# Optimization experiments

Hardware: AMD Instinct MI355X
Metric: run time of the kernel (lower is better)

## Reference

```python
import jax, jax.numpy as jnp
import numpy as np

B, C, H, W = 2, 256, 48, 48
KD = 256          # key_dim
CLS = 20          # num_classes
NT = H * W        # patch tokens in query
N = CLS + NT      # key length (cls tokens + patches)
HDS = 8           # num_heads
HD = C // HDS     # head_dim
SCALE = HD ** -0.5
MR = 0.3          # mask_ratio
EPS = 1e-5


def setup_inputs() -> dict:
    key = jax.random.key(0)
    ks = jax.random.split(key, 10)
    s = 0.02
    return {
        "x_query": jax.random.normal(ks[0], (B, C, H, W), jnp.float32),
        "x_key": jax.random.normal(ks[1], (B, N, KD), jnp.float32),
        "mask_u": jax.random.uniform(ks[2], (B, HDS, N, N), jnp.float32),
        "g1": jnp.ones((C,), jnp.float32), "be1": jnp.zeros((C,), jnp.float32),
        "g2": jnp.ones((KD,), jnp.float32), "be2": jnp.zeros((KD,), jnp.float32),
        "g3": jnp.ones((C,), jnp.float32), "be3": jnp.zeros((C,), jnp.float32),
        "Wq": jax.random.normal(ks[3], (C, C), jnp.float32) * s,
        "Wkv": jax.random.normal(ks[4], (KD, 2 * C), jnp.float32) * s,
        "Wcls": jax.random.normal(ks[5], (KD, C), jnp.float32) * s,
        "Wp": jax.random.normal(ks[6], (C, C), jnp.float32) * s,
        "bp": jnp.zeros((C,), jnp.float32),
        "W1": jax.random.normal(ks[7], (C, 4 * C), jnp.float32) * s,
        "bf1": jnp.zeros((4 * C,), jnp.float32),
        "W2": jax.random.normal(ks[8], (4 * C, C), jnp.float32) * s,
        "bf2": jnp.zeros((C,), jnp.float32),
    }


def _ln(x, g, b):
    m = jnp.mean(x, -1, keepdims=True)
    v = jnp.mean((x - m) ** 2, -1, keepdims=True)
    return (x - m) * jax.lax.rsqrt(v + EPS) * g + b


def reference(x_query, x_key, mask_u, g1, be1, g2, be2, g3, be3,
              Wq, Wkv, Wcls, Wp, bp, W1, bf1, W2, bf2):
    Bb, Cc, Hh, Ww = x_query.shape
    xq = x_query.transpose(0, 2, 3, 1).reshape(Bb, -1, Cc)  # [B, Nt, C]
    q_in = _ln(xq, g1, be1)
    k_in = _ln(x_key, g2, be2)
    # cross attention with cls-token prepend
    cls_t = k_in[:, :CLS] @ Wcls                      # [B, Cls, C]
    qcat = jnp.concatenate([cls_t, q_in @ Wq], 1)     # [B, Cls+Nt, C]
    M = qcat.shape[1]
    Nk = x_key.shape[1]
    q = qcat.reshape(Bb, M, HDS, HD).transpose(0, 2, 1, 3)        # [B,h,M,d]
    kv = (k_in @ Wkv).reshape(Bb, Nk, 2, HDS, HD).transpose(2, 0, 3, 1, 4)
    k, v = kv[0], kv[1]                                           # [B,h,N,d]
    attn = jnp.einsum('bhmd,bhnd->bhmn', q, k) * SCALE            # [B,h,M,N]
    # split softmax: cls columns and patch columns normalized separately
    attn = jnp.concatenate([
        jax.nn.softmax(attn[..., :CLS], axis=-1),
        jax.nn.softmax(attn[..., CLS:], axis=-1),
    ], axis=-1)
    # stochastic bernoulli(mask_ratio) mask -> -1e12, then re-softmax
    bern = (mask_u < MR).astype(attn.dtype)
    attn = jax.nn.softmax(attn + bern * (-1e12), axis=-1)
    x = jnp.einsum('bhmn,bhnd->bhmd', attn, v)
    x = x.transpose(0, 2, 1, 3).reshape(Bb, M, Cc)
    x = x @ Wp + bp
    x = x[:, CLS:]                                    # drop cls rows
    xq = xq + x                                       # residual 1
    h = jax.nn.gelu(_ln(xq, g3, be3) @ W1 + bf1, approximate=False)
    xq = xq + (h @ W2 + bf2)                          # residual 2 (MLP)
    return xq.transpose(0, 2, 1).reshape(Bb, Cc, Hh, Ww)
```

## Files before the change

### kernel.cpp

```cpp
#include <hip/hip_runtime.h>
#include <hip/hip_bf16.h>
#include <cstddef>

#define B_ 2
#define C_ 256
#define HW_ 2304
#define CLS_ 20
#define N_ 2324
#define HDS_ 8
#define HD_ 32
#define SCALE_F 0.17677669529663687f
#define MR_ 0.3f
#define EPS_ 1e-5f
#define NT64 37
#define NPAD 2368

typedef __attribute__((ext_vector_type(8))) short short8;
typedef __attribute__((ext_vector_type(4))) float f32x4;
typedef unsigned long long u64;

__device__ __forceinline__ short f2bf(float x) {
    union { __hip_bfloat16 b; short s; } u;
    u.b = __float2bfloat16(x);
    return u.s;
}
__device__ __forceinline__ u64 shfl_xor_u64(u64 v, int m) {
    unsigned lo = (unsigned)v, hi = (unsigned)(v >> 32);
    lo = (unsigned)__shfl_xor((int)lo, m, 64);
    hi = (unsigned)__shfl_xor((int)hi, m, 64);
    return ((u64)hi << 32) | lo;
}

__global__ __launch_bounds__(256) void wtrans_all_kernel(
    const float* __restrict__ Wq,  const float* __restrict__ Wkv,
    const float* __restrict__ Wp,  const float* __restrict__ W1,
    const float* __restrict__ W2,
    short* __restrict__ Wq_t, short* __restrict__ Wkv_t,
    short* __restrict__ Wp_t, short* __restrict__ W1_t,
    short* __restrict__ W2_t)
{
    __shared__ float S[32][33];
    int bid = blockIdx.x;
    const float* W; short* Wt; int K, Nn; float scale;
    if (bid < 64)       { W = Wq;  Wt = Wq_t;  K = 256;  Nn = 256;  scale = SCALE_F; }
    else if (bid < 192) { bid -= 64;  W = Wkv; Wt = Wkv_t; K = 256;  Nn = 512;  scale = 1.f; }
    else if (bid < 256) { bid -= 192; W = Wp;  Wt = Wp_t;  K = 256;  Nn = 256;  scale = 1.f; }
    else if (bid < 512) { bid -= 256; W = W1;  Wt = W1_t;  K = 256;  Nn = 1024; scale = 1.f; }
    else                { bid -= 512; W = W2;  Wt = W2_t;  K = 1024; Nn = 256;  scale = 1.f; }
    int nblk = Nn / 32;
    int n0 = (bid % nblk) * 32, k0 = (bid / nblk) * 32;
    int t = threadIdx.x;
    int nl = t & 31, kq = t >> 5;
    #pragma unroll
    for (int ii = 0; ii < 4; ++ii) {
        int k = kq + ii * 8;
        S[k][nl] = W[(size_t)(k0 + k) * Nn + n0 + nl] * scale;
    }
    __syncthreads();
    int kl = t & 31, nq = t >> 5;
    #pragma unroll
    for (int ii = 0; ii < 4; ++ii) {
        int n = nq + ii * 8;
        Wt[(size_t)(n0 + n) * K + k0 + kl] = f2bf(S[kl][n]);
    }
}

__global__ __launch_bounds__(256) void mask_compress_kernel(
    const float* __restrict__ mask, u64* __restrict__ mbits)
{
    int rid = blockIdx.x * 4 + (threadIdx.x >> 6);
    int l = threadIdx.x & 63;
    const float* mrow = mask + (size_t)rid * N_;
    u64* orow = mbits + (size_t)rid * NT64;
    float4 uu[10];
    #pragma unroll
    for (int base = 0; base < 10; ++base) {
        int col = base * 256 + l * 4;
        if (col < N_) uu[base] = *(const float4*)&mrow[col];
        else { uu[base].x = -1.f; uu[base].y = -1.f; uu[base].z = -1.f; uu[base].w = -1.f; }
    }
    #pragma unroll
    for (int base = 0; base < 10; ++base) {
        float4 u = uu[base];
        unsigned nib = (u.x >= MR_ ? 1u : 0u) | (u.y >= MR_ ? 2u : 0u)
                     | (u.z >= MR_ ? 4u : 0u) | (u.w >= MR_ ? 8u : 0u);
        u64 part = (u64)nib << (4 * (l & 15));
        part |= shfl_xor_u64(part, 1);
        part |= shfl_xor_u64(part, 2);
        part |= shfl_xor_u64(part, 4);
        part |= shfl_xor_u64(part, 8);
        int widx = base * 4 + (l >> 4);
        if ((l & 15) == 0 && widx < NT64) orow[widx] = part;
    }
}

__global__ __launch_bounds__(256) void lnq_kernel(
    const float* __restrict__ x, const float* __restrict__ g,
    const float* __restrict__ be, short* __restrict__ yln,
    float* __restrict__ yraw)
{
    int row = blockIdx.x;
    int b = row / HW_, n = row % HW_;
    int t = threadIdx.x;
    float v = x[((size_t)(b * C_ + t)) * HW_ + n];
    float s = v, s2 = v * v;
    #pragma unroll
    for (int off = 1; off < 64; off <<= 1) {
        s  += __shfl_xor(s,  off, 64);
        s2 += __shfl_xor(s2, off, 64);
    }
    __shared__ float rs[4], rs2[4];
    int w = t >> 6;
    if ((t & 63) == 0) { rs[w] = s; rs2[w] = s2; }
    __syncthreads();
    s  = rs[0] + rs[1] + rs[2] + rs[3];
    s2 = rs2[0] + rs2[1] + rs2[2] + rs2[3];
    float mean = s * (1.f / 256.f);
    float var  = s2 * (1.f / 256.f) - mean * mean;
    float inv  = rsqrtf(var + EPS_);
    yraw[(size_t)row * C_ + t] = v;
    yln [(size_t)row * C_ + t] = f2bf((v - mean) * inv * g[t] + be[t]);
}

__global__ __launch_bounds__(256) void ln_rows_kernel(
    const float* __restrict__ x, const float* __restrict__ g,
    const float* __restrict__ be, short* __restrict__ y)
{
    int row = blockIdx.x;
    int t = threadIdx.x;
    float v = x[(size_t)row * C_ + t];
    float s = v, s2 = v * v;
    #pragma unroll
    for (int off = 1; off < 64; off <<= 1) {
        s  += __shfl_xor(s,  off, 64);
        s2 += __shfl_xor(s2, off, 64);
    }
    __shared__ float rs[4], rs2[4];
    int w = t >> 6;
    if ((t & 63) == 0) { rs[w] = s; rs2[w] = s2; }
    __syncthreads();
    s  = rs[0] + rs[1] + rs[2] + rs[3];
    s2 = rs2[0] + rs2[1] + rs2[2] + rs2[3];
    float mean = s * (1.f / 256.f);
    float var  = s2 * (1.f / 256.f) - mean * mean;
    float inv  = rsqrtf(var + EPS_);
    y[(size_t)row * C_ + t] = f2bf((v - mean) * inv * g[t] + be[t]);
}

__global__ __launch_bounds__(256) void gemm_bf16_kernel(
    const short* __restrict__ A, const short* __restrict__ Wt,
    void* __restrict__ Cc, int M, int Nn, int K,
    const float* __restrict__ bias, const float* __restrict__ res, int flags)
{
    __shared__ short As[64][40];
    __shared__ short Ws[64][40];
    const int t = threadIdx.x, w = t >> 6, l = t & 63;
    const int quad = l >> 4, c16 = l & 15;
    const int m0 = blockIdx.y * 64, n0 = blockIdx.x * 64;
    const int wm = (w >> 1) * 32, wn = (w & 1) * 32;
    const int sr = t >> 2, sk = (t & 3) * 8;
    const f32x4 cz = {0.f, 0.f, 0.f, 0.f};
    f32x4 acc[2][2] = {{cz, cz}, {cz, cz}};
    int ga = m0 + sr; if (ga >= M) ga = M - 1;
    short8 av = *(const short8*)&A[(size_t)ga * K + sk];
    short8 wv = *(const short8*)&Wt[(size_t)(n0 + sr) * K + sk];
    for (int k0 = 0; k0 < K; k0 += 32) {
        __syncthreads();
        *(short8*)&As[sr][sk] = av;
        *(short8*)&Ws[sr][sk] = wv;
        if (k0 + 32 < K) {
            av = *(const short8*)&A[(size_t)ga * K + k0 + 32 + sk];
            wv = *(const short8*)&Wt[(size_t)(n0 + sr) * K + k0 + 32 + sk];
        }
        __syncthreads();
        short8 af0 = *(const short8*)&As[wm + c16][quad * 8];
        short8 af1 = *(const short8*)&As[wm + 16 + c16][quad * 8];
        short8 bf0 = *(const short8*)&Ws[wn + c16][quad * 8];
        short8 bf1 = *(const short8*)&Ws[wn + 16 + c16][quad * 8];
        acc[0][0] = __builtin_amdgcn_mfma_f32_16x16x32_bf16(af0, bf0, acc[0][0], 0, 0, 0);
        acc[0][1] = __builtin_amdgcn_mfma_f32_16x16x32_bf16(af0, bf1, acc[0][1], 0, 0, 0);
        acc[1][0] = __builtin_amdgcn_mfma_f32_16x16x32_bf16(af1, bf0, acc[1][0], 0, 0, 0);
        acc[1][1] = __builtin_amdgcn_mfma_f32_16x16x32_bf16(af1, bf1, acc[1][1], 0, 0, 0);
    }
    #pragma unroll
    for (int mb = 0; mb < 2; ++mb) {
        #pragma unroll
        for (int nb = 0; nb < 2; ++nb) {
            #pragma unroll
            for (int r = 0; r < 4; ++r) {
                int m = m0 + wm + mb * 16 + quad * 4 + r;
                if (m >= M) continue;
                int n = n0 + wn + nb * 16 + c16;
                float v = acc[mb][nb][r];
                if (bias) v += bias[n];
                if (flags & 1) v = 0.5f * v * (1.f + erff(v * 0.70710678118654752f));
                if (res) v += res[(size_t)m * Nn + n];
                if (flags & 2) ((short*)Cc)[(size_t)m * Nn + n] = f2bf(v);
                else           ((float*)Cc)[(size_t)m * Nn + n] = v;
            }
        }
    }
}

__global__ __launch_bounds__(256) void vtrans_kernel(
    const short* __restrict__ kvb, short* __restrict__ vtb)
{
    __shared__ short S[64][33];
    int n0 = blockIdx.x * 64;
    int bh = blockIdx.y;
    int b = bh >> 3, h = bh & 7;
    int t = threadIdx.x;
    int d = t & 31, i0 = t >> 5;
    #pragma unroll
    for (int ii = 0; ii < 8; ++ii) {
        int n = n0 + i0 + ii * 8;
        short v = 0;
        if (n < N_) v = kvb[((size_t)(b * N_ + n)) * 512 + 256 + h * 32 + d];
        S[i0 + ii * 8][d] = v;
    }
    __syncthreads();
    int nl = t & 63, d0 = t >> 6;
    #pragma unroll
    for (int jj = 0; jj < 8; ++jj) {
        int dd = d0 + jj * 4;
        vtb[(size_t)bh * 32 * NPAD + (size_t)dd * NPAD + n0 + nl] = S[nl][dd];
    }
}

__global__ __launch_bounds__(256) void attn_mfma_kernel(
    const short* __restrict__ qb,
    const short* __restrict__ kvb,
    const short* __restrict__ vtb,
    const u64*  __restrict__ mbits,
    short* __restrict__ ob)
{
    __shared__ short Ks[64][40];
    __shared__ short Vs[32][72];
    __shared__ short Ps[4][16][72];

    const int t = threadIdx.x;
    const int w = t >> 6, l = t & 63;
    const int quad = l >> 4, c16 = l & 15;
    const int bh = blockIdx.y;
    const int b = bh >> 3, h = bh & 7;
    const int mw = blockIdx.x * 64 + w * 16;
    const f32x4 cz = {0.f, 0.f, 0.f, 0.f};

    const short8 aq = *(const short8*)
        &qb[((size_t)(b * HW_ + mw + c16)) * C_ + h * HD_ + quad * 8];

    const int sn = t >> 2;
    const int sd = (t & 3) * 8;
    const int vd = t >> 3;
    const int vj = (t & 7) * 8;

    float l1[4] = {0.f, 0.f, 0.f, 0.f}, l2[4] = {0.f, 0.f, 0.f, 0.f};
    short8 kk = {0, 0, 0, 0, 0, 0, 0, 0};
    if (sn < N_)
        kk = *(const short8*)&kvb[((size_t)(b * N_ + sn)) * 512 + h * HD_ + sd];
    for (int j0 = 0; j0 < N_; j0 += 64) {
        __syncthreads();
        *(short8*)&Ks[sn][sd] = kk;
        if (j0 + 64 < N_) {
            int gn = j0 + 64 + sn;
            short8 nk = {0, 0, 0, 0, 0, 0, 0, 0};
            if (gn < N_)
                nk = *(const short8*)&kvb[((size_t)(b * N_ + gn)) * 512 + h * HD_ + sd];
            kk = nk;
        }
        __syncthreads();
        #pragma unroll
        for (int nb = 0; nb < 4; ++nb) {
            short8 bk = *(const short8*)&Ks[nb * 16 + c16][quad * 8];
            f32x4 c = __builtin_amdgcn_mfma_f32_16x16x32_bf16(aq, bk, cz, 0, 0, 0);
            int j = j0 + nb * 16 + c16;
            #pragma unroll
            for (int r = 0; r < 4; ++r) {
                float e = (j < N_) ? __expf(c[r]) : 0.f;
                if (j < CLS_) l1[r] += e; else l2[r] += e;
            }
        }
    }
    float i1[4], i2[4];
    #pragma unroll
    for (int r = 0; r < 4; ++r) {
        float a = l1[r], s = l2[r];
        #pragma unroll
        for (int off = 1; off < 16; off <<= 1) {
            a += __shfl_xor(a, off, 64);
            s += __shfl_xor(s, off, 64);
        }
        i1[r] = 1.f / a;
        i2[r] = 1.f / s;
    }

    f32x4 o0 = cz, o1 = cz;
    float zz[4] = {0.f, 0.f, 0.f, 0.f};
    const u64* mbase = mbits + ((size_t)bh * N_ + (CLS_ + mw + quad * 4)) * NT64;
    const size_t vrow = (size_t)bh * 32 * NPAD + (size_t)vd * NPAD + vj;
    short8 kk2 = {0, 0, 0, 0, 0, 0, 0, 0};
    if (sn < N_)
        kk2 = *(const short8*)&kvb[((size_t)(b * N_ + sn)) * 512 + h * HD_ + sd];
    short8 vv = *(const short8*)&vtb[vrow];
    for (int j0 = 0; j0 < N_; j0 += 64) {
        __syncthreads();
        *(short8*)&Ks[sn][sd] = kk2;
        *(short8*)&Vs[vd][vj] = vv;
        if (j0 + 64 < N_) {
            int gn = j0 + 64 + sn;
            short8 nk = {0, 0, 0, 0, 0, 0, 0, 0};
            if (gn < N_)
                nk = *(const short8*)&kvb[((size_t)(b * N_ + gn)) * 512 + h * HD_ + sd];
            kk2 = nk;
            vv = *(const short8*)&vtb[vrow + j0 + 64];
        }
        u64 wb[4];
        {
            const u64* mp = mbase + (j0 >> 6);
            #pragma unroll
            for (int r = 0; r < 4; ++r) wb[r] = mp[(size_t)r * NT64];
        }
        __syncthreads();
        #pragma unroll
        for (int nb = 0; nb < 4; ++nb) {
            short8 bk = *(const short8*)&Ks[nb * 16 + c16][quad * 8];
            f32x4 c = __builtin_amdgcn_mfma_f32_16x16x32_bf16(aq, bk, cz, 0, 0, 0);
            int j = j0 + nb * 16 + c16;
            #pragma unroll
            for (int r = 0; r < 4; ++r) {
                float iv = (j < CLS_) ? i1[r] : i2[r];
                float p = __expf(c[r]) * iv;
                bool keep = (wb[r] >> (nb * 16 + c16)) & 1;
                float wgt = keep ? __expf(p) : 0.f;
                zz[r] += wgt;
                Ps[w][quad * 4 + r][nb * 16 + c16] = f2bf(wgt);
            }
        }
        #pragma unroll
        for (int kc = 0; kc < 2; ++kc) {
            short8 ap  = *(const short8*)&Ps[w][c16][kc * 32 + quad * 8];
            short8 bv0 = *(const short8*)&Vs[c16][kc * 32 + quad * 8];
            short8 bv1 = *(const short8*)&Vs[16 + c16][kc * 32 + quad * 8];
            o0 = __builtin_amdgcn_mfma_f32_16x16x32_bf16(ap, bv0, o0, 0, 0, 0);
            o1 = __builtin_amdgcn_mfma_f32_16x16x32_bf16(ap, bv1, o1, 0, 0, 0);
        }
    }
    #pragma unroll
    for (int r = 0; r < 4; ++r) {
        float z = zz[r];
        #pragma unroll
        for (int off = 1; off < 16; off <<= 1) z += __shfl_xor(z, off, 64);
        float iz = 1.f / z;
        size_t orow = (size_t)(b * HW_ + mw + quad * 4 + r) * C_ + h * HD_;
        ob[orow + c16]      = f2bf(o0[r] * iz);
        ob[orow + 16 + c16] = f2bf(o1[r] * iz);
    }
}

__global__ __launch_bounds__(256) void transpose_kernel(
    const float* __restrict__ y, float* __restrict__ out)
{
    __shared__ float tile[64][65];
    int n0 = blockIdx.x * 64, c0 = blockIdx.y * 64, b = blockIdx.z;
    int lc = threadIdx.x & 63, lr = threadIdx.x >> 6;
    #pragma unroll
    for (int i = lr; i < 64; i += 4)
        tile[lc][i] = y[((size_t)(b * HW_ + n0 + i)) * C_ + c0 + lc];
    __syncthreads();
    #pragma unroll
    for (int i = lr; i < 64; i += 4)
        out[((size_t)(b * C_ + c0 + i)) * HW_ + n0 + lc] = tile[i][lc];
}

extern "C" void kernel_launch(void* const* d_in, const int* in_sizes, int n_in,
                              void* d_out, int out_size, void* d_ws, size_t ws_size,
                              hipStream_t stream)
{
    const float* x_query = (const float*)d_in[0];
    const float* x_key   = (const float*)d_in[1];
    const float* mask_u  = (const float*)d_in[2];
    const float* g1  = (const float*)d_in[3];
    const float* be1 = (const float*)d_in[4];
    const float* g2  = (const float*)d_in[5];
    const float* be2 = (const float*)d_in[6];
    const float* g3  = (const float*)d_in[7];
    const float* be3 = (const float*)d_in[8];
    const float* Wq  = (const float*)d_in[9];
    const float* Wkv = (const float*)d_in[10];
    const float* Wp  = (const float*)d_in[12];
    const float* bp  = (const float*)d_in[13];
    const float* W1  = (const float*)d_in[14];
    const float* bf1 = (const float*)d_in[15];
    const float* W2  = (const float*)d_in[16];
    const float* bf2 = (const float*)d_in[17];
    float* out = (float*)d_out;

    char* p = (char*)d_ws;
    short* Wq_t  = (short*)p; p += (size_t)256 * 256 * 2;
    short* Wkv_t = (short*)p; p += (size_t)512 * 256 * 2;
    short* Wp_t  = (short*)p; p += (size_t)256 * 256 * 2;
    short* W1_t  = (short*)p; p += (size_t)1024 * 256 * 2;
    short* W2_t  = (short*)p; p += (size_t)256 * 1024 * 2;
    u64*  mbits  = (u64*)p;   p += (size_t)16 * N_ * NT64 * 8;
    float* xq_t  = (float*)p; p += (size_t)B_ * HW_ * C_ * 4;
    short* q_in  = (short*)p; p += (size_t)B_ * HW_ * C_ * 2;
    short* k_in  = (short*)p; p += (size_t)B_ * N_ * C_ * 2;
    short* q_buf = (short*)p; p += (size_t)B_ * HW_ * C_ * 2;
    short* kv_b  = (short*)p; p += (size_t)B_ * N_ * 512 * 2;
    short* vt_b  = (short*)p; p += (size_t)16 * 32 * NPAD * 2;
    float* xq2   = (float*)p; p += (size_t)B_ * HW_ * C_ * 4;
    short* o_buf = q_in;
    short* ln3   = k_in;
    short* h_buf = (short*)mbits;
    float* y_buf = (float*)q_buf;

    wtrans_all_kernel<<<768, 256, 0, stream>>>(
        Wq, Wkv, Wp, W1, W2, Wq_t, Wkv_t, Wp_t, W1_t, W2_t);
    mask_compress_kernel<<<(16 * N_) / 4, 256, 0, stream>>>(mask_u, mbits);
    lnq_kernel<<<B_ * HW_, 256, 0, stream>>>(x_query, g1, be1, q_in, xq_t);
    ln_rows_kernel<<<B_ * N_, 256, 0, stream>>>(x_key, g2, be2, k_in);
    gemm_bf16_kernel<<<dim3(C_ / 64, (B_ * HW_) / 64), 256, 0, stream>>>(
        q_in, Wq_t, q_buf, B_ * HW_, C_, C_, nullptr, nullptr, 2);
    gemm_bf16_kernel<<<dim3(512 / 64, (B_ * N_ + 63) / 64), 256, 0, stream>>>(
        k_in, Wkv_t, kv_b, B_ * N_, 512, C_, nullptr, nullptr, 2);
    vtrans_kernel<<<dim3(NT64, 16), 256, 0, stream>>>(kv_b, vt_b);
    attn_mfma_kernel<<<dim3(HW_ / 64, B_ * HDS_), 256, 0, stream>>>(
        q_buf, kv_b, vt_b, mbits, o_buf);
    gemm_bf16_kernel<<<dim3(C_ / 64, (B_ * HW_) / 64), 256, 0, stream>>>(
        o_buf, Wp_t, xq2, B_ * HW_, C_, C_, bp, xq_t, 0);
    ln_rows_kernel<<<B_ * HW_, 256, 0, stream>>>(xq2, g3, be3, ln3);
    gemm_bf16_kernel<<<dim3(1024 / 64, (B_ * HW_) / 64), 256, 0, stream>>>(
        ln3, W1_t, h_buf, B_ * HW_, 1024, C_, bf1, nullptr, 3);
    gemm_bf16_kernel<<<dim3(C_ / 64, (B_ * HW_) / 64), 256, 0, stream>>>(
        h_buf, W2_t, y_buf, B_ * HW_, C_, 1024, bf2, xq2, 0);
    transpose_kernel<<<dim3(HW_ / 64, C_ / 64, B_), 256, 0, stream>>>(y_buf, out);
}
```

Baseline: 689.1 us.

## Fuse LN launches, widen GEMM K-tile, exp2 softmax, fold output transpose

Merges the query and key layernorm kernels into one launch. Doubles the GEMM K-tile to 64 so each block issues half as many syncs per K step. Pre-scales Wq by log2(e) so the attention kernel can use raw v_exp_f32, specialises the first and tail key tiles so per-element boundary checks are dropped, and prefetches mask words one tile ahead. The final GEMM now writes directly in NCHW layout, which removes the separate transpose kernel but makes that GEMM's output stores strided.

Result: faster. 663.6 us (-3.7%).

```diff
diff --git a/kernel.cpp b/kernel.cpp
--- a/kernel.cpp
+++ b/kernel.cpp
@@ -10,10 +10,13 @@
 #define HDS_ 8
 #define HD_ 32
 #define SCALE_F 0.17677669529663687f
+#define LOG2E_F 1.4426950408889634f
+#define QSCALE_F (SCALE_F * LOG2E_F)
 #define MR_ 0.3f
 #define EPS_ 1e-5f
 #define NT64 37
 #define NPAD 2368
+#define JTAIL 2304
 
 typedef __attribute__((ext_vector_type(8))) short short8;
 typedef __attribute__((ext_vector_type(4))) float f32x4;
@@ -23,6 +26,11 @@
     union { __hip_bfloat16 b; short s; } u;
     u.b = __float2bfloat16(x);
     return u.s;
+}
+__device__ __forceinline__ float fexp2(float x) {
+    float r;
+    asm volatile("v_exp_f32 %0, %1" : "=v"(r) : "v"(x));
+    return r;
 }
 __device__ __forceinline__ u64 shfl_xor_u64(u64 v, int m) {
     unsigned lo = (unsigned)v, hi = (unsigned)(v >> 32);
@@ -42,7 +50,7 @@
     __shared__ float S[32][33];
     int bid = blockIdx.x;
     const float* W; short* Wt; int K, Nn; float scale;
-    if (bid < 64)       { W = Wq;  Wt = Wq_t;  K = 256;  Nn = 256;  scale = SCALE_F; }
+    if (bid < 64)       { W = Wq;  Wt = Wq_t;  K = 256;  Nn = 256;  scale = QSCALE_F; }
     else if (bid < 192) { bid -= 64;  W = Wkv; Wt = Wkv_t; K = 256;  Nn = 512;  scale = 1.f; }
     else if (bid < 256) { bid -= 192; W = Wp;  Wt = Wp_t;  K = 256;  Nn = 256;  scale = 1.f; }
     else if (bid < 512) { bid -= 256; W = W1;  Wt = W1_t;  K = 256;  Nn = 1024; scale = 1.f; }
@@ -94,15 +102,23 @@
     }
 }
 
-__global__ __launch_bounds__(256) void lnq_kernel(
-    const float* __restrict__ x, const float* __restrict__ g,
-    const float* __restrict__ be, short* __restrict__ yln,
-    float* __restrict__ yraw)
+__global__ __launch_bounds__(256) void ln_qk_kernel(
+    const float* __restrict__ xq, const float* __restrict__ xk,
+    const float* __restrict__ g1, const float* __restrict__ be1,
+    const float* __restrict__ g2, const float* __restrict__ be2,
+    short* __restrict__ q_ln, float* __restrict__ q_raw,
+    short* __restrict__ k_ln)
 {
     int row = blockIdx.x;
-    int b = row / HW_, n = row % HW_;
     int t = threadIdx.x;
-    float v = x[((size_t)(b * C_ + t)) * HW_ + n];
+    bool isq = row < B_ * HW_;
+    float v;
+    if (isq) {
+        int b = row / HW_, n = row % HW_;
+        v = xq[((size_t)(b * C_ + t)) * HW_ + n];
+    } else {
+        v = xk[(size_t)(row - B_ * HW_) * C_ + t];
+    }
     float s = v, s2 = v * v;
     #pragma unroll
     for (int off = 1; off < 64; off <<= 1) {
@@ -118,8 +134,13 @@
     float mean = s * (1.f / 256.f);
     float var  = s2 * (1.f / 256.f) - mean * mean;
     float inv  = rsqrtf(var + EPS_);
-    yraw[(size_t)row * C_ + t] = v;
-    yln [(size_t)row * C_ + t] = f2bf((v - mean) * inv * g[t] + be[t]);
+    if (isq) {
+        q_raw[(size_t)row * C_ + t] = v;
+        q_ln [(size_t)row * C_ + t] = f2bf((v - mean) * inv * g1[t] + be1[t]);
+    } else {
+        k_ln[(size_t)(row - B_ * HW_) * C_ + t] =
+            f2bf((v - mean) * inv * g2[t] + be2[t]);
+    }
 }
 
 __global__ __launch_bounds__(256) void ln_rows_kernel(
@@ -152,35 +173,46 @@
     void* __restrict__ Cc, int M, int Nn, int K,
     const float* __restrict__ bias, const float* __restrict__ res, int flags)
 {
-    __shared__ short As[64][40];
-    __shared__ short Ws[64][40];
+    __shared__ short As[64][72];
+    __shared__ short Ws[64][72];
     const int t = threadIdx.x, w = t >> 6, l = t & 63;
     const int quad = l >> 4, c16 = l & 15;
     const int m0 = blockIdx.y * 64, n0 = blockIdx.x * 64;
     const int wm = (w >> 1) * 32, wn = (w & 1) * 32;
-    const int sr = t >> 2, sk = (t & 3) * 8;
+    const int sr = t >> 3;
+    const int sk = (t & 7) * 8;
     const f32x4 cz = {0.f, 0.f, 0.f, 0.f};
     f32x4 acc[2][2] = {{cz, cz}, {cz, cz}};
-    int ga = m0 + sr; if (ga >= M) ga = M - 1;
-    short8 av = *(const short8*)&A[(size_t)ga * K + sk];
-    short8 wv = *(const short8*)&Wt[(size_t)(n0 + sr) * K + sk];
-    for (int k0 = 0; k0 < K; k0 += 32) {
-        __syncthreads();
-        *(short8*)&As[sr][sk] = av;
-        *(short8*)&Ws[sr][sk] = wv;
-        if (k0 + 32 < K) {
-            av = *(const short8*)&A[(size_t)ga * K + k0 + 32 + sk];
-            wv = *(const short8*)&Wt[(size_t)(n0 + sr) * K + k0 + 32 + sk];
-        }
-        __syncthreads();
-        short8 af0 = *(const short8*)&As[wm + c16][quad * 8];
-        short8 af1 = *(const short8*)&As[wm + 16 + c16][quad * 8];
-        short8 bf0 = *(const short8*)&Ws[wn + c16][quad * 8];
-        short8 bf1 = *(const short8*)&Ws[wn + 16 + c16][quad * 8];
-        acc[0][0] = __builtin_amdgcn_mfma_f32_16x16x32_bf16(af0, bf0, acc[0][0], 0, 0, 0);
-        acc[0][1] = __builtin_amdgcn_mfma_f32_16x16x32_bf16(af0, bf1, acc[0][1], 0, 0, 0);
-        acc[1][0] = __builtin_amdgcn_mfma_f32_16x16x32_bf16(af1, bf0, acc[1][0], 0, 0, 0);
-        acc[1][1] = __builtin_amdgcn_mfma_f32_16x16x32_bf16(af1, bf1, acc[1][1], 0, 0, 0);
+    int ga0 = m0 + sr;      if (ga0 >= M) ga0 = M - 1;
+    int ga1 = m0 + 32 + sr; if (ga1 >= M) ga1 = M - 1;
+    short8 av0 = *(const short8*)&A[(size_t)ga0 * K + sk];
+    short8 av1 = *(const short8*)&A[(size_t)ga1 * K + sk];
+    short8 wv0 = *(const short8*)&Wt[(size_t)(n0 + sr) * K + sk];
+    short8 wv1 = *(const short8*)&Wt[(size_t)(n0 + 32 + sr) * K + sk];
+    for (int k0 = 0; k0 < K; k0 += 64) {
+        __syncthreads();
+        *(short8*)&As[sr][sk]      = av0;
+        *(short8*)&As[sr + 32][sk] = av1;
+        *(short8*)&Ws[sr][sk]      = wv0;
+        *(short8*)&Ws[sr + 32][sk] = wv1;
+        if (k0 + 64 < K) {
+            av0 = *(const short8*)&A[(size_t)ga0 * K + k0 + 64 + sk];
+            av1 = *(const short8*)&A[(size_t)ga1 * K + k0 + 64 + sk];
+            wv0 = *(const short8*)&Wt[(size_t)(n0 + sr) * K + k0 + 64 + sk];
+            wv1 = *(const short8*)&Wt[(size_t)(n0 + 32 + sr) * K + k0 + 64 + sk];
+        }
+        __syncthreads();
+        #pragma unroll
+        for (int kk = 0; kk < 2; ++kk) {
+            short8 af0 = *(const short8*)&As[wm + c16][kk * 32 + quad * 8];
+            short8 af1 = *(const short8*)&As[wm + 16 + c16][kk * 32 + quad * 8];
+            short8 bf0 = *(const short8*)&Ws[wn + c16][kk * 32 + quad * 8];
+            short8 bf1 = *(const short8*)&Ws[wn + 16 + c16][kk * 32 + quad * 8];
+            acc[0][0] = __builtin_amdgcn_mfma_f32_16x16x32_bf16(af0, bf0, acc[0][0], 0, 0, 0);
+            acc[0][1] = __builtin_amdgcn_mfma_f32_16x16x32_bf16(af0, bf1, acc[0][1], 0, 0, 0);
+            acc[1][0] = __builtin_amdgcn_mfma_f32_16x16x32_bf16(af1, bf0, acc[1][0], 0, 0, 0);
+            acc[1][1] = __builtin_amdgcn_mfma_f32_16x16x32_bf16(af1, bf1, acc[1][1], 0, 0, 0);
+        }
     }
     #pragma unroll
     for (int mb = 0; mb < 2; ++mb) {
@@ -195,8 +227,15 @@
                 if (bias) v += bias[n];
                 if (flags & 1) v = 0.5f * v * (1.f + erff(v * 0.70710678118654752f));
                 if (res) v += res[(size_t)m * Nn + n];
-                if (flags & 2) ((short*)Cc)[(size_t)m * Nn + n] = f2bf(v);
-                else           ((float*)Cc)[(size_t)m * Nn + n] = v;
+                if (flags & 4) {
+                    int bb = (m >= HW_) ? 1 : 0;
+                    int hw = m - bb * HW_;
+                    ((float*)Cc)[((size_t)(bb * Nn + n)) * HW_ + hw] = v;
+                } else if (flags & 2) {
+                    ((short*)Cc)[(size_t)m * Nn + n] = f2bf(v);
+                } else {
+                    ((float*)Cc)[(size_t)m * Nn + n] = v;
+                }
             }
         }
     }
@@ -255,9 +294,7 @@
     const int vj = (t & 7) * 8;
 
     float l1[4] = {0.f, 0.f, 0.f, 0.f}, l2[4] = {0.f, 0.f, 0.f, 0.f};
-    short8 kk = {0, 0, 0, 0, 0, 0, 0, 0};
-    if (sn < N_)
-        kk = *(const short8*)&kvb[((size_t)(b * N_ + sn)) * 512 + h * HD_ + sd];
+    short8 kk = *(const short8*)&kvb[((size_t)(b * N_ + sn)) * 512 + h * HD_ + sd];
     for (int j0 = 0; j0 < N_; j0 += 64) {
         __syncthreads();
         *(short8*)&Ks[sn][sd] = kk;
@@ -269,15 +306,38 @@
             kk = nk;
         }
         __syncthreads();
-        #pragma unroll
-        for (int nb = 0; nb < 4; ++nb) {
-            short8 bk = *(const short8*)&Ks[nb * 16 + c16][quad * 8];
-            f32x4 c = __builtin_amdgcn_mfma_f32_16x16x32_bf16(aq, bk, cz, 0, 0, 0);
-            int j = j0 + nb * 16 + c16;
-            #pragma unroll
-            for (int r = 0; r < 4; ++r) {
-                float e = (j < N_) ? __expf(c[r]) : 0.f;
-                if (j < CLS_) l1[r] += e; else l2[r] += e;
+        if (j0 == 0) {
+            #pragma unroll
+            for (int nb = 0; nb < 4; ++nb) {
+                short8 bk = *(const short8*)&Ks[nb * 16 + c16][quad * 8];
+                f32x4 c = __builtin_amdgcn_mfma_f32_16x16x32_bf16(aq, bk, cz, 0, 0, 0);
+                #pragma unroll
+                for (int r = 0; r < 4; ++r) {
+                    float e = fexp2(c[r]);
+                    if (nb == 0)      l1[r] += e;
+                    else if (nb == 1) { bool cl = c16 < 4; l1[r] += cl ? e : 0.f; l2[r] += cl ? 0.f : e; }
+                    else              l2[r] += e;
+                }
+            }
+        } else if (j0 == JTAIL) {
+            #pragma unroll
+            for (int nb = 0; nb < 2; ++nb) {
+                short8 bk = *(const short8*)&Ks[nb * 16 + c16][quad * 8];
+                f32x4 c = __builtin_amdgcn_mfma_f32_16x16x32_bf16(aq, bk, cz, 0, 0, 0);
+                #pragma unroll
+                for (int r = 0; r < 4; ++r) {
+                    float e = fexp2(c[r]);
+                    if (nb == 0) l2[r] += e;
+                    else         l2[r] += (c16 < 4) ? e : 0.f;
+                }
+            }
+        } else {
+            #pragma unroll
+            for (int nb = 0; nb < 4; ++nb) {
+                short8 bk = *(const short8*)&Ks[nb * 16 + c16][quad * 8];
+                f32x4 c = __builtin_amdgcn_mfma_f32_16x16x32_bf16(aq, bk, cz, 0, 0, 0);
+                #pragma unroll
+                for (int r = 0; r < 4; ++r) l2[r] += fexp2(c[r]);
             }
         }
     }
@@ -298,14 +358,18 @@
     float zz[4] = {0.f, 0.f, 0.f, 0.f};
     const u64* mbase = mbits + ((size_t)bh * N_ + (CLS_ + mw + quad * 4)) * NT64;
     const size_t vrow = (size_t)bh * 32 * NPAD + (size_t)vd * NPAD + vj;
-    short8 kk2 = {0, 0, 0, 0, 0, 0, 0, 0};
-    if (sn < N_)
-        kk2 = *(const short8*)&kvb[((size_t)(b * N_ + sn)) * 512 + h * HD_ + sd];
+    short8 kk2 = *(const short8*)&kvb[((size_t)(b * N_ + sn)) * 512 + h * HD_ + sd];
     short8 vv = *(const short8*)&vtb[vrow];
+    u64 wb[4];
+    #pragma unroll
+    for (int r = 0; r < 4; ++r) wb[r] = mbase[(size_t)r * NT64];
     for (int j0 = 0; j0 < N_; j0 += 64) {
         __syncthreads();
         *(short8*)&Ks[sn][sd] = kk2;
         *(short8*)&Vs[vd][vj] = vv;
+        u64 wbc[4];
+        #pragma unroll
+        for (int r = 0; r < 4; ++r) wbc[r] = wb[r];
         if (j0 + 64 < N_) {
             int gn = j0 + 64 + sn;
             short8 nk = {0, 0, 0, 0, 0, 0, 0, 0};
@@ -313,27 +377,42 @@
                 nk = *(const short8*)&kvb[((size_t)(b * N_ + gn)) * 512 + h * HD_ + sd];
             kk2 = nk;
             vv = *(const short8*)&vtb[vrow + j0 + 64];
-        }
-        u64 wb[4];
-        {
-            const u64* mp = mbase + (j0 >> 6);
+            const u64* mp = mbase + ((j0 + 64) >> 6);
             #pragma unroll
             for (int r = 0; r < 4; ++r) wb[r] = mp[(size_t)r * NT64];
         }
         __syncthreads();
-        #pragma unroll
-        for (int nb = 0; nb < 4; ++nb) {
-            short8 bk = *(const short8*)&Ks[nb * 16 + c16][quad * 8];
-            f32x4 c = __builtin_amdgcn_mfma_f32_16x16x32_bf16(aq, bk, cz, 0, 0, 0);
-            int j = j0 + nb * 16 + c16;
-            #pragma unroll
-            for (int r = 0; r < 4; ++r) {
-                float iv = (j < CLS_) ? i1[r] : i2[r];
-                float p = __expf(c[r]) * iv;
-                bool keep = (wb[r] >> (nb * 16 + c16)) & 1;
-                float wgt = keep ? __expf(p) : 0.f;
-                zz[r] += wgt;
-                Ps[w][quad * 4 + r][nb * 16 + c16] = f2bf(wgt);
+        if (j0 == 0) {
+            #pragma unroll
+            for (int nb = 0; nb < 4; ++nb) {
+                short8 bk = *(const short8*)&Ks[nb * 16 + c16][quad * 8];
+                f32x4 c = __builtin_amdgcn_mfma_f32_16x16x32_bf16(aq, bk, cz, 0, 0, 0);
+                #pragma unroll
+                for (int r = 0; r < 4; ++r) {
+                    float iv;
+                    if (nb == 0)      iv = i1[r];
+                    else if (nb == 1) iv = (c16 < 4) ? i1[r] : i2[r];
+                    else              iv = i2[r];
+                    float p = fexp2(c[r]) * iv;
+                    bool keep = (wbc[r] >> (nb * 16 + c16)) & 1;
+                    float wgt = keep ? fexp2(p * LOG2E_F) : 0.f;
+                    zz[r] += wgt;
+                    Ps[w][quad * 4 + r][nb * 16 + c16] = f2bf(wgt);
+                }
+            }
+        } else {
+            #pragma unroll
+            for (int nb = 0; nb < 4; ++nb) {
+                short8 bk = *(const short8*)&Ks[nb * 16 + c16][quad * 8];
+                f32x4 c = __builtin_amdgcn_mfma_f32_16x16x32_bf16(aq, bk, cz, 0, 0, 0);
+                #pragma unroll
+                for (int r = 0; r < 4; ++r) {
+                    float p = fexp2(c[r]) * i2[r];
+                    bool keep = (wbc[r] >> (nb * 16 + c16)) & 1;
+                    float wgt = keep ? fexp2(p * LOG2E_F) : 0.f;
+                    zz[r] += wgt;
+                    Ps[w][quad * 4 + r][nb * 16 + c16] = f2bf(wgt);
+                }
             }
         }
         #pragma unroll
@@ -355,21 +434,6 @@
         ob[orow + c16]      = f2bf(o0[r] * iz);
         ob[orow + 16 + c16] = f2bf(o1[r] * iz);
     }
-}
-
-__global__ __launch_bounds__(256) void transpose_kernel(
-    const float* __restrict__ y, float* __restrict__ out)
-{
-    __shared__ float tile[64][65];
-    int n0 = blockIdx.x * 64, c0 = blockIdx.y * 64, b = blockIdx.z;
-    int lc = threadIdx.x & 63, lr = threadIdx.x >> 6;
-    #pragma unroll
-    for (int i = lr; i < 64; i += 4)
-        tile[lc][i] = y[((size_t)(b * HW_ + n0 + i)) * C_ + c0 + lc];
-    __syncthreads();
-    #pragma unroll
-    for (int i = lr; i < 64; i += 4)
-        out[((size_t)(b * C_ + c0 + i)) * HW_ + n0 + lc] = tile[i][lc];
 }
 
 extern "C" void kernel_launch(void* const* d_in, const int* in_sizes, int n_in,
@@ -412,13 +476,12 @@
     short* o_buf = q_in;
     short* ln3   = k_in;
     short* h_buf = (short*)mbits;
-    float* y_buf = (float*)q_buf;
 
     wtrans_all_kernel<<<768, 256, 0, stream>>>(
         Wq, Wkv, Wp, W1, W2, Wq_t, Wkv_t, Wp_t, W1_t, W2_t);
     mask_compress_kernel<<<(16 * N_) / 4, 256, 0, stream>>>(mask_u, mbits);
-    lnq_kernel<<<B_ * HW_, 256, 0, stream>>>(x_query, g1, be1, q_in, xq_t);
-    ln_rows_kernel<<<B_ * N_, 256, 0, stream>>>(x_key, g2, be2, k_in);
+    ln_qk_kernel<<<B_ * HW_ + B_ * N_, 256, 0, stream>>>(
+        x_query, x_key, g1, be1, g2, be2, q_in, xq_t, k_in);
     gemm_bf16_kernel<<<dim3(C_ / 64, (B_ * HW_) / 64), 256, 0, stream>>>(
         q_in, Wq_t, q_buf, B_ * HW_, C_, C_, nullptr, nullptr, 2);
     gemm_bf16_kernel<<<dim3(512 / 64, (B_ * N_ + 63) / 64), 256, 0, stream>>>(
@@ -432,6 +495,5 @@
     gemm_bf16_kernel<<<dim3(1024 / 64, (B_ * HW_) / 64), 256, 0, stream>>>(
         ln3, W1_t, h_buf, B_ * HW_, 1024, C_, bf1, nullptr, 3);
     gemm_bf16_kernel<<<dim3(C_ / 64, (B_ * HW_) / 64), 256, 0, stream>>>(
-        h_buf, W2_t, y_buf, B_ * HW_, C_, 1024, bf2, xq2, 0);
-    transpose_kernel<<<dim3(HW_ / 64, C_ / 64, B_), 256, 0, stream>>>(y_buf, out);
-}
+        h_buf, W2_t, out, B_ * HW_, C_, 1024, bf2, xq2, 4);
+}
```
